# Kernel optimization log

Hardware: AMD Instinct MI355X
Metric: run time of the kernel (lower is better)

## Reference

```python
import jax, jax.numpy as jnp
import numpy as np

A_BITS = 4          # a_bits
W_BITS = 4          # w_bits / w_slices (w_slices = 1)
NUM_CHUNKS = 9      # ceil(in_ch*9 / 64) = ceil(576/64)
BN_EPS = 1e-5


def quantize_weight(w, bits):
    # WeightQuantize STE: uniform symmetric quantization, straight-through on clipped range
    n = 2.0 ** (bits - 1) - 1.0
    c = jnp.clip(w, -1.0, 1.0)
    q = jnp.round(c * n) / n
    return c + jax.lax.stop_gradient(q - c)


def create_input_stream(a, a_bits):
    # residual multi-bit binarization into a_bits sign planes, x ~= sum_i plane_i / 2^(i+1)
    x = jnp.clip(a, -1.0, 1.0)
    planes = []
    r = x
    for i in range(a_bits):
        s = jnp.where(r >= 0, 1.0, -1.0)
        planes.append(x + jax.lax.stop_gradient(s - x))  # STE plane
        r = r - s / (2.0 ** (i + 1))
    return jnp.stack(planes, 0)  # [a_bits, B, C*9, L]


def unfold3x3(x, pad=1):
    # torch F.unfold(kernel=3, stride=1) ordering: (C, kh, kw) flattened channel-major
    B, C, H, W = x.shape
    xp = jnp.pad(x, ((0, 0), (0, 0), (pad, pad), (pad, pad)))
    cols = jnp.stack([xp[:, :, i:i + H, j:j + W] for i in range(3) for j in range(3)], axis=2)
    return cols.reshape(B, C * 9, H * W)  # [B, C*9, L]


def mtj(x, gamma, beta, key):
    mean = x.mean(axis=(0, 2), keepdims=True)
    var = x.var(axis=(0, 2), keepdims=True)  # biased, as torch BN
    normed = (x - mean) / jnp.sqrt(var + BN_EPS) * gamma[None, :, None] + beta[None, :, None]
    t = jnp.tanh(4.0 * normed)
    rand = jax.random.uniform(key, x.shape, minval=-1.0, maxval=1.0)
    out = jnp.where(t > rand, 1.0, -1.0)
    out = jnp.where(normed == 0.0, 0.0, out)
    c = jnp.clip(normed, -1.0, 1.0)
    return c + jax.lax.stop_gradient(out - c)


def setup_inputs() -> dict:
    key = jax.random.key(0)
    k1, k2 = jax.random.split(key)
    inputs = jax.random.normal(k1, (8, 64, 32, 32), dtype=jnp.float32)
    weight = jax.random.normal(k2, (128, 64, 3, 3), dtype=jnp.float32) * (2.0 / (64 * 9)) ** 0.5
    gamma = jnp.ones((128,), jnp.float32)
    beta = jnp.zeros((128,), jnp.float32)
    return {"inputs": inputs, "weight": weight, "gamma": gamma, "beta": beta}


def reference(inputs, weight, gamma, beta):
    O = weight.shape[0]
    # weight standardization (per output filter; std is unbiased as torch .std())
    wf = weight.reshape(O, -1)
    bw = weight - wf.mean(-1)[:, None, None, None]
    std = bw.reshape(O, -1).std(-1, ddof=1)
    bw = bw / std[:, None, None, None]
    qw = quantize_weight(bw, W_BITS)                      # [O, C, 3, 3]
    a = unfold3x3(inputs)                                 # [B, C*9, L]
    stream = create_input_stream(a, A_BITS)               # [A, B, C*9, L]
    A, B, CK, L = stream.shape
    cs = CK // NUM_CHUNKS
    x = stream.reshape(A * B, NUM_CHUNKS, cs, L)          # chunked along the C*9 axis
    fw = qw.reshape(O, NUM_CHUNKS, cs)                    # flattened weight chunks
    # per-chunk F.linear, vectorized over chunks: [nc, A*B, O, L]
    lt = jnp.einsum('ngkl,ogk->gnol', x, fw)
    keys = jax.random.split(jax.random.key(42), NUM_CHUNKS)
    pre = jax.vmap(lambda t, k: mtj(t, gamma, beta, k))(lt, keys) / NUM_CHUNKS
    out = pre.sum(0)                                      # sum chunks (w_slices=1 -> identity combine)
    # gen_image_vector_and_sum: recombine activation bit-planes
    out = out.reshape(A, B, O, L)
    wts = (2.0 ** -(jnp.arange(A, dtype=jnp.float32) + 1.0)).reshape(A, 1, 1, 1)
    out = (out * wts).sum(0)
    HW = int(np.sqrt(L))
    return out.reshape(B, O, HW, HW)                      # F.fold with (1,1) kernel
```

## Files before the change

### kernel.cpp

```cpp
#include <hip/hip_runtime.h>
#include <stdint.h>

#ifndef PRNG_PARTITIONABLE
#define PRNG_PARTITIONABLE 1
#endif

#define ONE_M_U 0.99999994039535522461f

__device__ __forceinline__ void tf_4a(uint32_t& x0, uint32_t& x1){
  x0 += x1; x1 = (x1<<13)|(x1>>19); x1 ^= x0;
  x0 += x1; x1 = (x1<<15)|(x1>>17); x1 ^= x0;
  x0 += x1; x1 = (x1<<26)|(x1>>6);  x1 ^= x0;
  x0 += x1; x1 = (x1<<6) |(x1>>26); x1 ^= x0;
}
__device__ __forceinline__ void tf_4b(uint32_t& x0, uint32_t& x1){
  x0 += x1; x1 = (x1<<17)|(x1>>15); x1 ^= x0;
  x0 += x1; x1 = (x1<<29)|(x1>>3);  x1 ^= x0;
  x0 += x1; x1 = (x1<<16)|(x1>>16); x1 ^= x0;
  x0 += x1; x1 = (x1<<24)|(x1>>8);  x1 ^= x0;
}
__device__ __forceinline__ void threefry2x32(uint32_t k0, uint32_t k1, uint32_t& x0, uint32_t& x1){
  uint32_t k2 = k0 ^ k1 ^ 0x1BD11BDAu;
  x0 += k0; x1 += k1;
  tf_4a(x0,x1); x0 += k1; x1 += k2 + 1u;
  tf_4b(x0,x1); x0 += k2; x1 += k0 + 2u;
  tf_4a(x0,x1); x0 += k0; x1 += k1 + 3u;
  tf_4b(x0,x1); x0 += k1; x1 += k2 + 4u;
  tf_4a(x0,x1); x0 += k2; x1 += k0 + 5u;
}

__device__ __forceinline__ float bits_to_unit(uint32_t b){
  #pragma clang fp contract(off)
  float f = __uint_as_float((b >> 9) | 0x3f800000u) - 1.0f;
  float r = f * 2.0f + (-1.0f);
  return __builtin_fmaxf(-1.0f, r);
}

__device__ __forceinline__ float xla_tanh_f32(float x){
  #pragma clang fp contract(off)
  float ax = __builtin_fabsf(x);
  float xc = __builtin_fminf(__builtin_fmaxf(x, -9.0f), 9.0f);
  float x2 = xc * xc;
  float nm = -2.76076847742355e-16f;
  nm = x2 * nm + 2.00018790482477e-13f;
  nm = x2 * nm + -8.60467152213735e-11f;
  nm = x2 * nm + 5.12229709037114e-08f;
  nm = x2 * nm + 1.48572235717979e-05f;
  nm = x2 * nm + 6.37261928875436e-04f;
  nm = x2 * nm + 4.89352455891786e-03f;
  nm = xc * nm;
  float dn = 1.19825839466702e-06f;
  dn = x2 * dn + 1.18534705686654e-04f;
  dn = x2 * dn + 2.26843463243900e-03f;
  dn = x2 * dn + 4.89352518554385e-03f;
  float res = nm / dn;
  return (ax < 0.0004f) ? x : res;
}

__device__ __forceinline__ float rfl_f(float v){
  return __uint_as_float(__builtin_amdgcn_readfirstlane(__float_as_uint(v)));
}

__device__ __forceinline__ float dot64(unsigned long long sw, unsigned long long dw,
                                       const float* w){
  float acc = 0.0f;
  #pragma unroll
  for (int k = 0; k < 64; ++k){
    float mag = ((dw >> k) & 1ull) ? ONE_M_U : 1.0f;
    float p   = ((sw >> k) & 1ull) ? mag : -mag;
    acc = __builtin_fmaf(p, w[k], acc);
  }
  return acc;
}

#define QW_OFF   0u
#define SGN_OFF  294912u
#define DIM_OFF  2654208u
#define KEYS_OFF 5013504u
#define MV_OFF   5013632u
#define LT_OFF   5023744u
#define LT_BYTES 150994944u
#define PART_OFF (LT_OFF + LT_BYTES)
#define PART_BYTES 2359296u
#define PART2_OFF (PART_OFF + PART_BYTES)
#define PART2_BYTES 73728u
#define WS_NEEDED_FAST (PART2_OFF + PART2_BYTES)

__global__ __launch_bounds__(64) void k_weights(const float* __restrict__ W,
        float* __restrict__ qw, uint32_t* __restrict__ keys){
  #pragma clang fp contract(off)
  __shared__ float  bwL[576];
  __shared__ double red[64];
  int o = blockIdx.x, t = threadIdx.x;
  double s = 0.0;
  for (int j = t; j < 576; j += 64) s += (double)W[o*576 + j];
  red[t] = s; __syncthreads();
  for (int k = 32; k > 0; k >>= 1){ if (t < k) red[t] += red[t+k]; __syncthreads(); }
  float mean1 = (float)(red[0] / 576.0);
  __syncthreads();
  for (int j = t; j < 576; j += 64) bwL[j] = W[o*576 + j] - mean1;
  __syncthreads();
  s = 0.0;
  for (int j = t; j < 576; j += 64) s += (double)bwL[j];
  red[t] = s; __syncthreads();
  for (int k = 32; k > 0; k >>= 1){ if (t < k) red[t] += red[t+k]; __syncthreads(); }
  float mean2 = (float)(red[0] / 576.0);
  __syncthreads();
  s = 0.0;
  for (int j = t; j < 576; j += 64){ float c = bwL[j] - mean2; float sq = c * c; s += (double)sq; }
  red[t] = s; __syncthreads();
  for (int k = 32; k > 0; k >>= 1){ if (t < k) red[t] += red[t+k]; __syncthreads(); }
  float varf = (float)(red[0] / 575.0);
  float stdv = __builtin_sqrtf(varf);
  __syncthreads();
  for (int j = t; j < 576; j += 64){
    float b2 = bwL[j] / stdv;
    float c  = __builtin_fminf(__builtin_fmaxf(b2, -1.0f), 1.0f);
    float q  = __builtin_rintf(c * 7.0f) / 7.0f;
    float fwd = c + (q - c);
    int g = j >> 6, k = j & 63;
    qw [(g*128 + o)*64 + k] = fwd;
  }
  if (o == 0 && t == 0){
#if PRNG_PARTITIONABLE
    for (int g = 0; g < 9; ++g){
      uint32_t x0 = 0u, x1 = (uint32_t)g;
      threefry2x32(0u, 42u, x0, x1);
      keys[2*g] = x0; keys[2*g+1] = x1;
    }
#else
    uint32_t outv[18];
    for (int i = 0; i < 9; ++i){
      uint32_t x0 = (uint32_t)i, x1 = (uint32_t)(9 + i);
      threefry2x32(0u, 42u, x0, x1);
      outv[i] = x0; outv[9+i] = x1;
    }
    for (int j = 0; j < 18; ++j) keys[j] = outv[j];
#endif
  }
}

__global__ __launch_bounds__(256) void k_stream(const float* __restrict__ X,
        unsigned long long* __restrict__ sgn, unsigned long long* __restrict__ dimw){
  #pragma clang fp contract(off)
  int g = blockIdx.y;
  int tid = blockIdx.x * 256 + threadIdx.x;
  int b = tid >> 10, l = tid & 1023;
  int h = l >> 5, w = l & 31;
  unsigned long long sw0=0ull, sw1=0ull, sw2=0ull, sw3=0ull;
  unsigned long long dw0=0ull, dw1=0ull, dw2=0ull, dw3=0ull;
  const float* Xb = X + b*64*1024;
  int ck0 = g*64;
  #pragma unroll
  for (int i = 0; i < 64; ++i){
    int ck = ck0 + i;
    int c = ck / 9, kp = ck % 9;
    int di = kp / 3 - 1, dj = kp % 3 - 1;
    int hh = h + di, ww = w + dj;
    float v = 0.0f;
    if (hh >= 0 && hh < 32 && ww >= 0 && ww < 32)
      v = Xb[(c*32 + hh)*32 + ww];
    float x = __builtin_fminf(__builtin_fmaxf(v, -1.0f), 1.0f);
    float r = x;
    {
      float sv = (r >= 0.0f) ? 1.0f : -1.0f;
      float d  = sv - x; float p = x + d;
      if (sv > 0.0f) sw0 |= (1ull << i);
      if (__builtin_fabsf(p) < 1.0f) dw0 |= (1ull << i);
      r = r - sv * 0.5f;
    }
    {
      float sv = (r >= 0.0f) ? 1.0f : -1.0f;
      float d  = sv - x; float p = x + d;
      if (sv > 0.0f) sw1 |= (1ull << i);
      if (__builtin_fabsf(p) < 1.0f) dw1 |= (1ull << i);
      r = r - sv * 0.25f;
    }
    {
      float sv = (r >= 0.0f) ? 1.0f : -1.0f;
      float d  = sv - x; float p = x + d;
      if (sv > 0.0f) sw2 |= (1ull << i);
      if (__builtin_fabsf(p) < 1.0f) dw2 |= (1ull << i);
      r = r - sv * 0.125f;
    }
    {
      float sv = (r >= 0.0f) ? 1.0f : -1.0f;
      float d  = sv - x; float p = x + d;
      if (sv > 0.0f) sw3 |= (1ull << i);
      if (__builtin_fabsf(p) < 1.0f) dw3 |= (1ull << i);
      r = r - sv * 0.0625f;
    }
  }
  sgn [((0*8+b)*9 + g)*1024 + l] = sw0;
  sgn [((1*8+b)*9 + g)*1024 + l] = sw1;
  sgn [((2*8+b)*9 + g)*1024 + l] = sw2;
  sgn [((3*8+b)*9 + g)*1024 + l] = sw3;
  dimw[((0*8+b)*9 + g)*1024 + l] = dw0;
  dimw[((1*8+b)*9 + g)*1024 + l] = dw1;
  dimw[((2*8+b)*9 + g)*1024 + l] = dw2;
  dimw[((3*8+b)*9 + g)*1024 + l] = dw3;
}

__global__ __launch_bounds__(256) void k_gemm(const float* __restrict__ qw,
        const unsigned long long* __restrict__ sgn, const unsigned long long* __restrict__ dimw,
        float* __restrict__ lt, double* __restrict__ part){
  __shared__ float4 wS[128*17];
  __shared__ float4 pS[128*17];
  int lq = blockIdx.x, g = blockIdx.y, n = blockIdx.z;
  int t = threadIdx.x;
  {
    int o = t >> 4, kq = t & 15;
    const float4* qw4 = (const float4*)qw;
    #pragma unroll
    for (int i = 0; i < 8; ++i){
      int oo = o + 16*i;
      wS[oo*17 + kq] = qw4[(g*128 + oo)*16 + kq];
    }
  }
  {
    int l = t >> 1, kh = t & 1;
    unsigned long long sw = sgn [(n*9+g)*1024 + lq*128 + l];
    unsigned long long dw = dimw[(n*9+g)*1024 + lq*128 + l];
    #pragma unroll
    for (int kq = 0; kq < 8; ++kq){
      int kqq = kh*8 + kq;
      float4 v;
      {
        int k = kqq*4;
        float m0 = ((dw>>k)&1ull)?ONE_M_U:1.0f; v.x = ((sw>>k)&1ull)?m0:-m0;
        float m1 = ((dw>>(k+1))&1ull)?ONE_M_U:1.0f; v.y = ((sw>>(k+1))&1ull)?m1:-m1;
        float m2 = ((dw>>(k+2))&1ull)?ONE_M_U:1.0f; v.z = ((sw>>(k+2))&1ull)?m2:-m2;
        float m3 = ((dw>>(k+3))&1ull)?ONE_M_U:1.0f; v.w = ((sw>>(k+3))&1ull)?m3:-m3;
      }
      pS[l*17 + kqq] = v;
    }
  }
  __syncthreads();
  int ot = t >> 4, ltl = t & 15;
  float acc[8][8];
  #pragma unroll
  for (int i = 0; i < 8; ++i)
    #pragma unroll
    for (int j = 0; j < 8; ++j) acc[i][j] = 0.0f;
  for (int kq = 0; kq < 16; ++kq){
    float wr[8][4], pr[8][4];
    #pragma unroll
    for (int i = 0; i < 8; ++i) *(float4*)wr[i] = wS[(ot*8+i)*17 + kq];
    #pragma unroll
    for (int j = 0; j < 8; ++j) *(float4*)pr[j] = pS[(ltl+16*j)*17 + kq];
    #pragma unroll
    for (int e = 0; e < 4; ++e)
      #pragma unroll
      for (int i = 0; i < 8; ++i)
        #pragma unroll
        for (int j = 0; j < 8; ++j)
          acc[i][j] = __builtin_fmaf(pr[j][e], wr[i][e], acc[i][j]);
  }
  #pragma unroll
  for (int i = 0; i < 8; ++i){
    int o = ot*8 + i;
    float* dst = lt + ((size_t)((n*9+g)*128 + o))*1024 + lq*128 + ltl;
    #pragma unroll
    for (int j = 0; j < 8; ++j) dst[16*j] = acc[i][j];
  }
  double ps[8];
  #pragma unroll
  for (int i = 0; i < 8; ++i){
    double s = 0.0;
    #pragma unroll
    for (int j = 0; j < 8; ++j) s += (double)acc[i][j];
    ps[i] = s;
  }
  __syncthreads();
  double* red = (double*)pS;
  #pragma unroll
  for (int i = 0; i < 8; ++i) red[(ot*8+i)*16 + ltl] = ps[i];
  __syncthreads();
  if (t < 128){
    double s = 0.0;
    #pragma unroll
    for (int q = 0; q < 16; ++q) s += red[t*16 + q];
    part[((size_t)g*128 + t)*256 + n*8 + lq] = s;
  }
}

__global__ __launch_bounds__(256) void k_stats2a(const float* __restrict__ lt,
        const double* __restrict__ part, float* __restrict__ mv,
        double* __restrict__ part2){
  #pragma clang fp contract(off)
  __shared__ double redm[64];
  __shared__ double red[256];
  __shared__ float meanS;
  int go = blockIdx.x;
  int g = go >> 7, o = go & 127;
  int ns = blockIdx.y, t = threadIdx.x;
  if (t < 64){
    double s = 0.0;
    for (int idx = t; idx < 256; idx += 64) s += part[(size_t)go*256 + idx];
    redm[t] = s;
  }
  __syncthreads();
  for (int k = 32; k > 0; k >>= 1){ if (t < k) redm[t] += redm[t+k]; __syncthreads(); }
  if (t == 0){
    float mean = (float)(redm[0] / 32768.0);
    if (ns == 0) mv[go*2] = mean;
    meanS = mean;
  }
  __syncthreads();
  float mean = meanS;
  double s2 = 0.0;
  for (int n = ns*4; n < ns*4 + 4; ++n){
    const float4* p4 = (const float4*)(lt + ((size_t)((n*9+g)*128 + o)) * 1024);
    float4 v = p4[t];
    { float c = v.x - mean; float sq = c * c; s2 += (double)sq; }
    { float c = v.y - mean; float sq = c * c; s2 += (double)sq; }
    { float c = v.z - mean; float sq = c * c; s2 += (double)sq; }
    { float c = v.w - mean; float sq = c * c; s2 += (double)sq; }
  }
  red[t] = s2; __syncthreads();
  for (int k = 128; k > 0; k >>= 1){ if (t < k) red[t] += red[t+k]; __syncthreads(); }
  if (t == 0) part2[go*8 + ns] = red[0];
}

__global__ __launch_bounds__(256) void k_den(const double* __restrict__ part2,
        float* __restrict__ mv){
  int go = blockIdx.x*256 + threadIdx.x;
  if (go >= 1152) return;
  double s = 0.0;
  #pragma unroll
  for (int ns = 0; ns < 8; ++ns) s += part2[go*8 + ns];
  float var = (float)(s / 32768.0);
  mv[go*2 + 1] = __builtin_sqrtf(var + 1e-5f);
}

__global__ __launch_bounds__(256) void k_out_fast(const float* __restrict__ lt,
        const float* __restrict__ mv, const uint32_t* __restrict__ keys,
        const float* __restrict__ gamma, const float* __restrict__ beta,
        float* __restrict__ out){
  #pragma clang fp contract(off)
  int bi = blockIdx.x;
  int lc = bi & 3, o = (bi >> 2) & 127, b = bi >> 9;
  int t = threadIdx.x;
  int l = lc*256 + t;
  float gma = rfl_f(gamma[o]), bta = rfl_f(beta[o]);
  uint32_t kk0[9], kk1[9];
  float mg[9], dg[9];
  #pragma unroll
  for (int g = 0; g < 9; ++g){
    kk0[g] = __builtin_amdgcn_readfirstlane(keys[2*g]);
    kk1[g] = __builtin_amdgcn_readfirstlane(keys[2*g+1]);
    mg[g]  = rfl_f(mv[(g*128+o)*2]);
    dg[g]  = rfl_f(mv[(g*128+o)*2+1]);
  }
  float tv[4][9];
  const float* pb = lt + ((size_t)(b*9*128 + o))*1024 + l;
  #pragma unroll
  for (int a = 0; a < 4; ++a)
    #pragma unroll
    for (int g = 0; g < 9; ++g)
      tv[a][g] = pb[(size_t)(a*72 + g)*131072];
  float S[4];
  #pragma unroll
  for (int a = 0; a < 4; ++a){
    float Sa = 0.0f;
#if PRNG_PARTITIONABLE
    uint32_t m = (uint32_t)((a*8 + b)*131072 + o*1024 + l);
#endif
    #pragma unroll
    for (int g = 0; g < 9; ++g){
      float rnd;
#if PRNG_PARTITIONABLE
      uint32_t x0 = 0u, x1 = m;
      threefry2x32(kk0[g], kk1[g], x0, x1);
      rnd = bits_to_unit(x0 ^ x1);
#else
      uint32_t mm = (uint32_t)(((a&1)*8 + b)*131072 + o*1024 + l);
      uint32_t x0 = mm, x1 = mm + 2097152u;
      threefry2x32(kk0[g], kk1[g], x0, x1);
      rnd = (a < 2) ? bits_to_unit(x0) : bits_to_unit(x1);
#endif
      float normed = (tv[a][g] - mg[g]) / dg[g] * gma + bta;
      float th = xla_tanh_f32(4.0f * normed);
      float dec = (th > rnd) ? 1.0f : -1.0f;
      if (normed == 0.0f) dec = 0.0f;
      float cc  = __builtin_fminf(__builtin_fmaxf(normed, -1.0f), 1.0f);
      float fwd = cc + (dec - cc);
      float pre = fwd / 9.0f;
      Sa = Sa + pre;
    }
    S[a] = Sa;
  }
  float z = S[0] * 0.5f;
  z = z + S[1] * 0.25f;
  z = z + S[2] * 0.125f;
  z = z + S[3] * 0.0625f;
  out[(b*128 + o)*1024 + l] = z;
}

__global__ __launch_bounds__(256) void k_stats_slow(const float* __restrict__ qw,
        const unsigned long long* __restrict__ sgn, const unsigned long long* __restrict__ dimw,
        float* __restrict__ mv){
  #pragma clang fp contract(off)
  __shared__ double red[256];
  int g = blockIdx.x >> 7, o = blockIdx.x & 127, t = threadIdx.x;
  float wr[64];
  #pragma unroll
  for (int k = 0; k < 64; ++k) wr[k] = qw[(g*128 + o)*64 + k];
  double s1 = 0.0;
  for (int n = 0; n < 32; ++n){
    const unsigned long long* sp = sgn  + (n*9 + g)*1024;
    const unsigned long long* dp = dimw + (n*9 + g)*1024;
    for (int j = 0; j < 4; ++j){
      int l = t + j*256;
      float tvv = dot64(sp[l], dp[l], wr);
      s1 += (double)tvv;
    }
  }
  red[t] = s1; __syncthreads();
  for (int k = 128; k > 0; k >>= 1){ if (t < k) red[t] += red[t+k]; __syncthreads(); }
  float mean = (float)(red[0] / 32768.0);
  __syncthreads();
  double s2 = 0.0;
  for (int n = 0; n < 32; ++n){
    const unsigned long long* sp = sgn  + (n*9 + g)*1024;
    const unsigned long long* dp = dimw + (n*9 + g)*1024;
    for (int j = 0; j < 4; ++j){
      int l = t + j*256;
      float tvv = dot64(sp[l], dp[l], wr);
      float c = tvv - mean;
      float sq = c * c;
      s2 += (double)sq;
    }
  }
  red[t] = s2; __syncthreads();
  for (int k = 128; k > 0; k >>= 1){ if (t < k) red[t] += red[t+k]; __syncthreads(); }
  if (t == 0){
    float var = (float)(red[0] / 32768.0);
    float den = __builtin_sqrtf(var + 1e-5f);
    mv[(g*128+o)*2]   = mean;
    mv[(g*128+o)*2+1] = den;
  }
}

__global__ __launch_bounds__(256) void k_out_slow(const float* __restrict__ qw,
        const unsigned long long* __restrict__ sgn, const unsigned long long* __restrict__ dimw,
        const float* __restrict__ mv, const uint32_t* __restrict__ keys,
        const float* __restrict__ gamma, const float* __restrict__ beta,
        float* __restrict__ out){
  #pragma clang fp contract(off)
  __shared__ float    wv[576];
  __shared__ float    mvL[18];
  __shared__ uint32_t kL[18];
  int bi = blockIdx.x;
  int lc = bi & 3, o = (bi >> 2) & 127, b = bi >> 9;
  int t = threadIdx.x;
  for (int j = t; j < 576; j += 256) wv[j] = qw[((j >> 6)*128 + o)*64 + (j & 63)];
  if (t < 18){ mvL[t] = mv[((t>>1)*128 + o)*2 + (t&1)]; kL[t] = keys[t]; }
  __syncthreads();
  int l = lc*256 + t;
  float gma = gamma[o], bta = beta[o];
  float S[4] = {0.0f, 0.0f, 0.0f, 0.0f};
  for (int g = 0; g < 9; ++g){
    float rnd[4];
#if PRNG_PARTITIONABLE
    #pragma unroll
    for (int a = 0; a < 4; ++a){
      uint32_t m = (uint32_t)((a*8 + b)*131072 + o*1024 + l);
      uint32_t x0 = 0u, x1 = m;
      threefry2x32(kL[2*g], kL[2*g+1], x0, x1);
      rnd[a] = bits_to_unit(x0 ^ x1);
    }
#else
    #pragma unroll
    for (int a01 = 0; a01 < 2; ++a01){
      uint32_t m = (uint32_t)((a01*8 + b)*131072 + o*1024 + l);
      uint32_t x0 = m, x1 = m + 2097152u;
      threefry2x32(kL[2*g], kL[2*g+1], x0, x1);
      rnd[a01]     = bits_to_unit(x0);
      rnd[a01 + 2] = bits_to_unit(x1);
    }
#endif
    float mean = mvL[2*g], den = mvL[2*g+1];
    float wr[64];
    #pragma unroll
    for (int k = 0; k < 64; ++k) wr[k] = wv[g*64 + k];
    #pragma unroll
    for (int a = 0; a < 4; ++a){
      int n = a*8 + b;
      float tvv = dot64(sgn[(n*9+g)*1024 + l], dimw[(n*9+g)*1024 + l], wr);
      float normed = (tvv - mean) / den * gma + bta;
      float th = xla_tanh_f32(4.0f * normed);
      float dec = (th > rnd[a]) ? 1.0f : -1.0f;
      if (normed == 0.0f) dec = 0.0f;
      float cc  = __builtin_fminf(__builtin_fmaxf(normed, -1.0f), 1.0f);
      float fwd = cc + (dec - cc);
      float pre = fwd / 9.0f;
      S[a] = S[a] + pre;
    }
  }
  float z = S[0] * 0.5f;
  z = z + S[1] * 0.25f;
  z = z + S[2] * 0.125f;
  z = z + S[3] * 0.0625f;
  out[(b*128 + o)*1024 + l] = z;
}

extern "C" void kernel_launch(void* const* d_in, const int* in_sizes, int n_in,
                              void* d_out, int out_size, void* d_ws, size_t ws_size,
                              hipStream_t stream){
  (void)in_sizes; (void)n_in; (void)out_size;
  const float* inp   = (const float*)d_in[0];
  const float* wgt   = (const float*)d_in[1];
  const float* gamma = (const float*)d_in[2];
  const float* beta  = (const float*)d_in[3];
  float* out = (float*)d_out;
  char* ws = (char*)d_ws;
  float*              qw    = (float*)(ws + QW_OFF);
  unsigned long long* sgn   = (unsigned long long*)(ws + SGN_OFF);
  unsigned long long* dimw  = (unsigned long long*)(ws + DIM_OFF);
  uint32_t*           keys  = (uint32_t*)(ws + KEYS_OFF);
  float*              mv    = (float*)(ws + MV_OFF);
  float*              lt    = (float*)(ws + LT_OFF);
  double*             part  = (double*)(ws + PART_OFF);
  double*             part2 = (double*)(ws + PART2_OFF);

  hipLaunchKernelGGL(k_weights, dim3(128),    dim3(64),  0, stream, wgt, qw, keys);
  hipLaunchKernelGGL(k_stream,  dim3(32, 9),  dim3(256), 0, stream, inp, sgn, dimw);
  if (ws_size >= (size_t)WS_NEEDED_FAST){
    hipLaunchKernelGGL(k_gemm,     dim3(8, 9, 32), dim3(256), 0, stream, qw, sgn, dimw, lt, part);
    hipLaunchKernelGGL(k_stats2a,  dim3(1152, 8),  dim3(256), 0, stream, lt, part, mv, part2);
    hipLaunchKernelGGL(k_den,      dim3(5),        dim3(256), 0, stream, part2, mv);
    hipLaunchKernelGGL(k_out_fast, dim3(4096),     dim3(256), 0, stream, lt, mv, keys,
                       gamma, beta, out);
  } else {
    hipLaunchKernelGGL(k_stats_slow, dim3(1152), dim3(256), 0, stream, qw, sgn, dimw, mv);
    hipLaunchKernelGGL(k_out_slow,   dim3(4096), dim3(256), 0, stream, qw, sgn, dimw, mv, keys,
                       gamma, beta, out);
  }
}
```

Baseline: 330.5 us.

## Merge front kernels, fold variance reduction into one kernel, restructure output loop

Weight quantization and input bit-plane stream kernels are merged into one launch with block-index dispatch. The split variance kernel and its finalize kernel are collapsed into a single kernel that loops over all samples per (g,o), removing the part2 buffer and a launch. The output kernel now stages per-o means and keys in shared memory and interleaves chunk loops so loads of lt are done incrementally rather than holding 36 values in registers. This trades fewer launches and lower register pressure for less parallelism in the stats kernel (1152 blocks instead of 9216).

```diff
diff --git a/kernel.cpp b/kernel.cpp
--- a/kernel.cpp
+++ b/kernel.cpp
@@ -57,10 +57,6 @@
   return (ax < 0.0004f) ? x : res;
 }
 
-__device__ __forceinline__ float rfl_f(float v){
-  return __uint_as_float(__builtin_amdgcn_readfirstlane(__float_as_uint(v)));
-}
-
 __device__ __forceinline__ float dot64(unsigned long long sw, unsigned long long dw,
                                        const float* w){
   float acc = 0.0f;
@@ -82,123 +78,131 @@
 #define LT_BYTES 150994944u
 #define PART_OFF (LT_OFF + LT_BYTES)
 #define PART_BYTES 2359296u
-#define PART2_OFF (PART_OFF + PART_BYTES)
-#define PART2_BYTES 73728u
-#define WS_NEEDED_FAST (PART2_OFF + PART2_BYTES)
-
-__global__ __launch_bounds__(64) void k_weights(const float* __restrict__ W,
-        float* __restrict__ qw, uint32_t* __restrict__ keys){
+#define WS_NEEDED_FAST (PART_OFF + PART_BYTES)
+
+__global__ __launch_bounds__(256) void k_front(const float* __restrict__ X,
+        const float* __restrict__ W, float* __restrict__ qw, uint32_t* __restrict__ keys,
+        unsigned long long* __restrict__ sgn, unsigned long long* __restrict__ dimw){
   #pragma clang fp contract(off)
   __shared__ float  bwL[576];
   __shared__ double red[64];
-  int o = blockIdx.x, t = threadIdx.x;
-  double s = 0.0;
-  for (int j = t; j < 576; j += 64) s += (double)W[o*576 + j];
-  red[t] = s; __syncthreads();
-  for (int k = 32; k > 0; k >>= 1){ if (t < k) red[t] += red[t+k]; __syncthreads(); }
-  float mean1 = (float)(red[0] / 576.0);
-  __syncthreads();
-  for (int j = t; j < 576; j += 64) bwL[j] = W[o*576 + j] - mean1;
-  __syncthreads();
-  s = 0.0;
-  for (int j = t; j < 576; j += 64) s += (double)bwL[j];
-  red[t] = s; __syncthreads();
-  for (int k = 32; k > 0; k >>= 1){ if (t < k) red[t] += red[t+k]; __syncthreads(); }
-  float mean2 = (float)(red[0] / 576.0);
-  __syncthreads();
-  s = 0.0;
-  for (int j = t; j < 576; j += 64){ float c = bwL[j] - mean2; float sq = c * c; s += (double)sq; }
-  red[t] = s; __syncthreads();
-  for (int k = 32; k > 0; k >>= 1){ if (t < k) red[t] += red[t+k]; __syncthreads(); }
-  float varf = (float)(red[0] / 575.0);
-  float stdv = __builtin_sqrtf(varf);
-  __syncthreads();
-  for (int j = t; j < 576; j += 64){
-    float b2 = bwL[j] / stdv;
-    float c  = __builtin_fminf(__builtin_fmaxf(b2, -1.0f), 1.0f);
-    float q  = __builtin_rintf(c * 7.0f) / 7.0f;
-    float fwd = c + (q - c);
-    int g = j >> 6, k = j & 63;
-    qw [(g*128 + o)*64 + k] = fwd;
-  }
-  if (o == 0 && t == 0){
+  int bx = blockIdx.x;
+  int t = threadIdx.x;
+  if (bx < 288){
+    int g = bx >> 5;
+    int tid = (bx & 31) * 256 + t;
+    int b = tid >> 10, l = tid & 1023;
+    int h = l >> 5, w = l & 31;
+    unsigned long long sw0=0ull, sw1=0ull, sw2=0ull, sw3=0ull;
+    unsigned long long dw0=0ull, dw1=0ull, dw2=0ull, dw3=0ull;
+    const float* Xb = X + b*64*1024;
+    int ck0 = g*64;
+    #pragma unroll
+    for (int i = 0; i < 64; ++i){
+      int ck = ck0 + i;
+      int c = ck / 9, kp = ck % 9;
+      int di = kp / 3 - 1, dj = kp % 3 - 1;
+      int hh = h + di, ww = w + dj;
+      float v = 0.0f;
+      if (hh >= 0 && hh < 32 && ww >= 0 && ww < 32)
+        v = Xb[(c*32 + hh)*32 + ww];
+      float x = __builtin_fminf(__builtin_fmaxf(v, -1.0f), 1.0f);
+      float r = x;
+      {
+        float sv = (r >= 0.0f) ? 1.0f : -1.0f;
+        float d  = sv - x; float p = x + d;
+        if (sv > 0.0f) sw0 |= (1ull << i);
+        if (__builtin_fabsf(p) < 1.0f) dw0 |= (1ull << i);
+        r = r - sv * 0.5f;
+      }
+      {
+        float sv = (r >= 0.0f) ? 1.0f : -1.0f;
+        float d  = sv - x; float p = x + d;
+        if (sv > 0.0f) sw1 |= (1ull << i);
+        if (__builtin_fabsf(p) < 1.0f) dw1 |= (1ull << i);
+        r = r - sv * 0.25f;
+      }
+      {
+        float sv = (r >= 0.0f) ? 1.0f : -1.0f;
+        float d  = sv - x; float p = x + d;
+        if (sv > 0.0f) sw2 |= (1ull << i);
+        if (__builtin_fabsf(p) < 1.0f) dw2 |= (1ull << i);
+        r = r - sv * 0.125f;
+      }
+      {
+        float sv = (r >= 0.0f) ? 1.0f : -1.0f;
+        float d  = sv - x; float p = x + d;
+        if (sv > 0.0f) sw3 |= (1ull << i);
+        if (__builtin_fabsf(p) < 1.0f) dw3 |= (1ull << i);
+        r = r - sv * 0.0625f;
+      }
+    }
+    sgn [((0*8+b)*9 + g)*1024 + l] = sw0;
+    sgn [((1*8+b)*9 + g)*1024 + l] = sw1;
+    sgn [((2*8+b)*9 + g)*1024 + l] = sw2;
+    sgn [((3*8+b)*9 + g)*1024 + l] = sw3;
+    dimw[((0*8+b)*9 + g)*1024 + l] = dw0;
+    dimw[((1*8+b)*9 + g)*1024 + l] = dw1;
+    dimw[((2*8+b)*9 + g)*1024 + l] = dw2;
+    dimw[((3*8+b)*9 + g)*1024 + l] = dw3;
+  } else {
+    int o = bx - 288;
+    if (t < 64){
+      double s = 0.0;
+      for (int j = t; j < 576; j += 64) s += (double)W[o*576 + j];
+      red[t] = s;
+    }
+    __syncthreads();
+    for (int k = 32; k > 0; k >>= 1){ if (t < k) red[t] += red[t+k]; __syncthreads(); }
+    float mean1 = (float)(red[0] / 576.0);
+    __syncthreads();
+    for (int j = t; j < 576; j += 256) bwL[j] = W[o*576 + j] - mean1;
+    __syncthreads();
+    if (t < 64){
+      double s = 0.0;
+      for (int j = t; j < 576; j += 64) s += (double)bwL[j];
+      red[t] = s;
+    }
+    __syncthreads();
+    for (int k = 32; k > 0; k >>= 1){ if (t < k) red[t] += red[t+k]; __syncthreads(); }
+    float mean2 = (float)(red[0] / 576.0);
+    __syncthreads();
+    if (t < 64){
+      double s = 0.0;
+      for (int j = t; j < 576; j += 64){ float c = bwL[j] - mean2; float sq = c * c; s += (double)sq; }
+      red[t] = s;
+    }
+    __syncthreads();
+    for (int k = 32; k > 0; k >>= 1){ if (t < k) red[t] += red[t+k]; __syncthreads(); }
+    float varf = (float)(red[0] / 575.0);
+    float stdv = __builtin_sqrtf(varf);
+    __syncthreads();
+    for (int j = t; j < 576; j += 256){
+      float b2 = bwL[j] / stdv;
+      float c  = __builtin_fminf(__builtin_fmaxf(b2, -1.0f), 1.0f);
+      float q  = __builtin_rintf(c * 7.0f) / 7.0f;
+      float fwd = c + (q - c);
+      int g = j >> 6, k = j & 63;
+      qw [(g*128 + o)*64 + k] = fwd;
+    }
+    if (o == 0 && t == 0){
 #if PRNG_PARTITIONABLE
-    for (int g = 0; g < 9; ++g){
-      uint32_t x0 = 0u, x1 = (uint32_t)g;
-      threefry2x32(0u, 42u, x0, x1);
-      keys[2*g] = x0; keys[2*g+1] = x1;
-    }
+      for (int g = 0; g < 9; ++g){
+        uint32_t x0 = 0u, x1 = (uint32_t)g;
+        threefry2x32(0u, 42u, x0, x1);
+        keys[2*g] = x0; keys[2*g+1] = x1;
+      }
 #else
-    uint32_t outv[18];
-    for (int i = 0; i < 9; ++i){
-      uint32_t x0 = (uint32_t)i, x1 = (uint32_t)(9 + i);
-      threefry2x32(0u, 42u, x0, x1);
-      outv[i] = x0; outv[9+i] = x1;
-    }
-    for (int j = 0; j < 18; ++j) keys[j] = outv[j];
+      uint32_t outv[18];
+      for (int i = 0; i < 9; ++i){
+        uint32_t x0 = (uint32_t)i, x1 = (uint32_t)(9 + i);
+        threefry2x32(0u, 42u, x0, x1);
+        outv[i] = x0; outv[9+i] = x1;
+      }
+      for (int j = 0; j < 18; ++j) keys[j] = outv[j];
 #endif
-  }
-}
-
-__global__ __launch_bounds__(256) void k_stream(const float* __restrict__ X,
-        unsigned long long* __restrict__ sgn, unsigned long long* __restrict__ dimw){
-  #pragma clang fp contract(off)
-  int g = blockIdx.y;
-  int tid = blockIdx.x * 256 + threadIdx.x;
-  int b = tid >> 10, l = tid & 1023;
-  int h = l >> 5, w = l & 31;
-  unsigned long long sw0=0ull, sw1=0ull, sw2=0ull, sw3=0ull;
-  unsigned long long dw0=0ull, dw1=0ull, dw2=0ull, dw3=0ull;
-  const float* Xb = X + b*64*1024;
-  int ck0 = g*64;
-  #pragma unroll
-  for (int i = 0; i < 64; ++i){
-    int ck = ck0 + i;
-    int c = ck / 9, kp = ck % 9;
-    int di = kp / 3 - 1, dj = kp % 3 - 1;
-    int hh = h + di, ww = w + dj;
-    float v = 0.0f;
-    if (hh >= 0 && hh < 32 && ww >= 0 && ww < 32)
-      v = Xb[(c*32 + hh)*32 + ww];
-    float x = __builtin_fminf(__builtin_fmaxf(v, -1.0f), 1.0f);
-    float r = x;
-    {
-      float sv = (r >= 0.0f) ? 1.0f : -1.0f;
-      float d  = sv - x; float p = x + d;
-      if (sv > 0.0f) sw0 |= (1ull << i);
-      if (__builtin_fabsf(p) < 1.0f) dw0 |= (1ull << i);
-      r = r - sv * 0.5f;
-    }
-    {
-      float sv = (r >= 0.0f) ? 1.0f : -1.0f;
-      float d  = sv - x; float p = x + d;
-      if (sv > 0.0f) sw1 |= (1ull << i);
-      if (__builtin_fabsf(p) < 1.0f) dw1 |= (1ull << i);
-      r = r - sv * 0.25f;
-    }
-    {
-      float sv = (r >= 0.0f) ? 1.0f : -1.0f;
-      float d  = sv - x; float p = x + d;
-      if (sv > 0.0f) sw2 |= (1ull << i);
-      if (__builtin_fabsf(p) < 1.0f) dw2 |= (1ull << i);
-      r = r - sv * 0.125f;
-    }
-    {
-      float sv = (r >= 0.0f) ? 1.0f : -1.0f;
-      float d  = sv - x; float p = x + d;
-      if (sv > 0.0f) sw3 |= (1ull << i);
-      if (__builtin_fabsf(p) < 1.0f) dw3 |= (1ull << i);
-      r = r - sv * 0.0625f;
-    }
-  }
-  sgn [((0*8+b)*9 + g)*1024 + l] = sw0;
-  sgn [((1*8+b)*9 + g)*1024 + l] = sw1;
-  sgn [((2*8+b)*9 + g)*1024 + l] = sw2;
-  sgn [((3*8+b)*9 + g)*1024 + l] = sw3;
-  dimw[((0*8+b)*9 + g)*1024 + l] = dw0;
-  dimw[((1*8+b)*9 + g)*1024 + l] = dw1;
-  dimw[((2*8+b)*9 + g)*1024 + l] = dw2;
-  dimw[((3*8+b)*9 + g)*1024 + l] = dw3;
+    }
+  }
 }
 
 __global__ __launch_bounds__(256) void k_gemm(const float* __restrict__ qw,
@@ -284,16 +288,15 @@
   }
 }
 
-__global__ __launch_bounds__(256) void k_stats2a(const float* __restrict__ lt,
-        const double* __restrict__ part, float* __restrict__ mv,
-        double* __restrict__ part2){
+__global__ __launch_bounds__(256) void k_stats(const float* __restrict__ lt,
+        const double* __restrict__ part, float* __restrict__ mv){
   #pragma clang fp contract(off)
   __shared__ double redm[64];
   __shared__ double red[256];
   __shared__ float meanS;
   int go = blockIdx.x;
   int g = go >> 7, o = go & 127;
-  int ns = blockIdx.y, t = threadIdx.x;
+  int t = threadIdx.x;
   if (t < 64){
     double s = 0.0;
     for (int idx = t; idx < 256; idx += 64) s += part[(size_t)go*256 + idx];
@@ -303,34 +306,31 @@
   for (int k = 32; k > 0; k >>= 1){ if (t < k) redm[t] += redm[t+k]; __syncthreads(); }
   if (t == 0){
     float mean = (float)(redm[0] / 32768.0);
-    if (ns == 0) mv[go*2] = mean;
+    mv[go*2] = mean;
     meanS = mean;
   }
   __syncthreads();
   float mean = meanS;
-  double s2 = 0.0;
-  for (int n = ns*4; n < ns*4 + 4; ++n){
-    const float4* p4 = (const float4*)(lt + ((size_t)((n*9+g)*128 + o)) * 1024);
-    float4 v = p4[t];
-    { float c = v.x - mean; float sq = c * c; s2 += (double)sq; }
-    { float c = v.y - mean; float sq = c * c; s2 += (double)sq; }
-    { float c = v.z - mean; float sq = c * c; s2 += (double)sq; }
-    { float c = v.w - mean; float sq = c * c; s2 += (double)sq; }
-  }
-  red[t] = s2; __syncthreads();
-  for (int k = 128; k > 0; k >>= 1){ if (t < k) red[t] += red[t+k]; __syncthreads(); }
-  if (t == 0) part2[go*8 + ns] = red[0];
-}
-
-__global__ __launch_bounds__(256) void k_den(const double* __restrict__ part2,
-        float* __restrict__ mv){
-  int go = blockIdx.x*256 + threadIdx.x;
-  if (go >= 1152) return;
-  double s = 0.0;
-  #pragma unroll
-  for (int ns = 0; ns < 8; ++ns) s += part2[go*8 + ns];
-  float var = (float)(s / 32768.0);
-  mv[go*2 + 1] = __builtin_sqrtf(var + 1e-5f);
+  double total = 0.0;
+  for (int ns = 0; ns < 8; ++ns){
+    double s2 = 0.0;
+    for (int n = ns*4; n < ns*4 + 4; ++n){
+      const float4* p4 = (const float4*)(lt + ((size_t)((n*9+g)*128 + o)) * 1024);
+      float4 v = p4[t];
+      { float c = v.x - mean; float sq = c * c; s2 += (double)sq; }
+      { float c = v.y - mean; float sq = c * c; s2 += (double)sq; }
+      { float c = v.z - mean; float sq = c * c; s2 += (double)sq; }
+      { float c = v.w - mean; float sq = c * c; s2 += (double)sq; }
+    }
+    __syncthreads();
+    red[t] = s2; __syncthreads();
+    for (int k = 128; k > 0; k >>= 1){ if (t < k) red[t] += red[t+k]; __syncthreads(); }
+    if (t == 0) total += red[0];
+  }
+  if (t == 0){
+    float var = (float)(total / 32768.0);
+    mv[go*2 + 1] = __builtin_sqrtf(var + 1e-5f);
+  }
 }
 
 __global__ __launch_bounds__(256) void k_out_fast(const float* __restrict__ lt,
@@ -338,57 +338,50 @@
         const float* __restrict__ gamma, const float* __restrict__ beta,
         float* __restrict__ out){
   #pragma clang fp contract(off)
+  __shared__ float    mvL[18];
+  __shared__ uint32_t kL[18];
   int bi = blockIdx.x;
   int lc = bi & 3, o = (bi >> 2) & 127, b = bi >> 9;
   int t = threadIdx.x;
+  if (t < 18){ mvL[t] = mv[((t>>1)*128 + o)*2 + (t&1)]; kL[t] = keys[t]; }
+  __syncthreads();
   int l = lc*256 + t;
-  float gma = rfl_f(gamma[o]), bta = rfl_f(beta[o]);
-  uint32_t kk0[9], kk1[9];
-  float mg[9], dg[9];
-  #pragma unroll
+  float gma = gamma[o], bta = beta[o];
+  float S[4] = {0.0f, 0.0f, 0.0f, 0.0f};
   for (int g = 0; g < 9; ++g){
-    kk0[g] = __builtin_amdgcn_readfirstlane(keys[2*g]);
-    kk1[g] = __builtin_amdgcn_readfirstlane(keys[2*g+1]);
-    mg[g]  = rfl_f(mv[(g*128+o)*2]);
-    dg[g]  = rfl_f(mv[(g*128+o)*2+1]);
-  }
-  float tv[4][9];
-  const float* pb = lt + ((size_t)(b*9*128 + o))*1024 + l;
-  #pragma unroll
-  for (int a = 0; a < 4; ++a)
-    #pragma unroll
-    for (int g = 0; g < 9; ++g)
-      tv[a][g] = pb[(size_t)(a*72 + g)*131072];
-  float S[4];
-  #pragma unroll
-  for (int a = 0; a < 4; ++a){
-    float Sa = 0.0f;
+    float rnd[4];
 #if PRNG_PARTITIONABLE
-    uint32_t m = (uint32_t)((a*8 + b)*131072 + o*1024 + l);
+    #pragma unroll
+    for (int a = 0; a < 4; ++a){
+      uint32_t m = (uint32_t)((a*8 + b)*131072 + o*1024 + l);
+      uint32_t x0 = 0u, x1 = m;
+      threefry2x32(kL[2*g], kL[2*g+1], x0, x1);
+      rnd[a] = bits_to_unit(x0 ^ x1);
+    }
+#else
+    #pragma unroll
+    for (int a01 = 0; a01 < 2; ++a01){
+      uint32_t m = (uint32_t)((a01*8 + b)*131072 + o*1024 + l);
+      uint32_t x0 = m, x1 = m + 2097152u;
+      threefry2x32(kL[2*g], kL[2*g+1], x0, x1);
+      rnd[a01]     = bits_to_unit(x0);
+      rnd[a01 + 2] = bits_to_unit(x1);
+    }
 #endif
-    #pragma unroll
-    for (int g = 0; g < 9; ++g){
-      float rnd;
-#if PRNG_PARTITIONABLE
-      uint32_t x0 = 0u, x1 = m;
-      threefry2x32(kk0[g], kk1[g], x0, x1);
-      rnd = bits_to_unit(x0 ^ x1);
-#else
-      uint32_t mm = (uint32_t)(((a&1)*8 + b)*131072 + o*1024 + l);
-      uint32_t x0 = mm, x1 = mm + 2097152u;
-      threefry2x32(kk0[g], kk1[g], x0, x1);
-      rnd = (a < 2) ? bits_to_unit(x0) : bits_to_unit(x1);
-#endif
-      float normed = (tv[a][g] - mg[g]) / dg[g] * gma + bta;
+    float mean = mvL[2*g], den = mvL[2*g+1];
+    #pragma unroll
+    for (int a = 0; a < 4; ++a){
+      int n = a*8 + b;
+      float tv = lt[((size_t)((n*9+g)*128 + o)) * 1024 + l];
+      float normed = (tv - mean) / den * gma + bta;
       float th = xla_tanh_f32(4.0f * normed);
-      float dec = (th > rnd) ? 1.0f : -1.0f;
+      float dec = (th > rnd[a]) ? 1.0f : -1.0f;
       if (normed == 0.0f) dec = 0.0f;
       float cc  = __builtin_fminf(__builtin_fmaxf(normed, -1.0f), 1.0f);
       float fwd = cc + (dec - cc);
       float pre = fwd / 9.0f;
-      Sa = Sa + pre;
-    }
-    S[a] = Sa;
+      S[a] = S[a] + pre;
+    }
   }
   float z = S[0] * 0.5f;
   z = z + S[1] * 0.25f;
@@ -522,14 +515,11 @@
   float*              mv    = (float*)(ws + MV_OFF);
   float*              lt    = (float*)(ws + LT_OFF);
   double*             part  = (double*)(ws + PART_OFF);
-  double*             part2 = (double*)(ws + PART2_OFF);
-
-  hipLaunchKernelGGL(k_weights, dim3(128),    dim3(64),  0, stream, wgt, qw, keys);
-  hipLaunchKernelGGL(k_stream,  dim3(32, 9),  dim3(256), 0, stream, inp, sgn, dimw);
+
+  hipLaunchKernelGGL(k_front, dim3(416), dim3(256), 0, stream, inp, wgt, qw, keys, sgn, dimw);
   if (ws_size >= (size_t)WS_NEEDED_FAST){
     hipLaunchKernelGGL(k_gemm,     dim3(8, 9, 32), dim3(256), 0, stream, qw, sgn, dimw, lt, part);
-    hipLaunchKernelGGL(k_stats2a,  dim3(1152, 8),  dim3(256), 0, stream, lt, part, mv, part2);
-    hipLaunchKernelGGL(k_den,      dim3(5),        dim3(256), 0, stream, part2, mv);
+    hipLaunchKernelGGL(k_stats,    dim3(1152),     dim3(256), 0, stream, lt, part, mv);
     hipLaunchKernelGGL(k_out_fast, dim3(4096),     dim3(256), 0, stream, lt, mv, keys,
                        gamma, beta, out);
   } else {
```

Result: faster. 284.4 us (-13.9%).
